# Kernel tuning notes

Hardware: AMD Instinct MI355X
Metric: run time of the kernel (lower is better)

The kernel has to match this reference:

```python
import jax, jax.numpy as jnp
import numpy as np

N = 20000    # num nodes
E = 320000   # num edges (also rows of edge_type, SPN line-graph style)
F = 64       # num_features
HID = 64     # hidden_channels
HEADS = 4    # gatv2_heads
NC = 2       # num_classes
PH = 128     # proxy hidden size
SLOPE = 0.2  # PyG GATv2 leaky_relu negative slope


def gatv2(feat, src, dst, wl, wr, att, b, num_nodes, concat):
    # GATv2Conv (PyG semantics, add_self_loops=True, dropout off in eval)
    H, C = att.shape
    xl = (feat @ wl).reshape(-1, H, C)
    xr = (feat @ wr).reshape(-1, H, C)
    loops = jnp.arange(num_nodes, dtype=src.dtype)
    s = jnp.concatenate([src, loops])
    d = jnp.concatenate([dst, loops])
    e = jax.nn.leaky_relu(xl[s] + xr[d], SLOPE)            # [E', H, C]
    logits = jnp.einsum('ehc,hc->eh', e, att)              # [E', H]
    m = jax.ops.segment_max(logits, d, num_segments=num_nodes)
    p = jnp.exp(logits - m[d])
    z = jax.ops.segment_sum(p, d, num_segments=num_nodes)
    alpha = p / z[d]                                       # segment softmax
    out = jax.ops.segment_sum(xl[s] * alpha[:, :, None], d, num_segments=num_nodes)
    out = out.reshape(num_nodes, H * C) if concat else out.mean(axis=1)
    return out + b


def setup_inputs():
    key = jax.random.key(0)
    ks = iter(jax.random.split(key, 32))
    def rn(shape, scale=0.1):
        return jax.random.normal(next(ks), shape, dtype=jnp.float32) * scale
    return {
        'x': rn((N, F), 1.0),
        'edge_type': rn((E, F), 1.0),
        'edge_index': jax.random.randint(next(ks), (2, E), 0, N, dtype=jnp.int32),
        'n1_wl': rn((F, HEADS * HID)), 'n1_wr': rn((F, HEADS * HID)),
        'n1_att': rn((HEADS, HID)), 'n1_b': jnp.zeros((HEADS * HID,), jnp.float32),
        'n2_wl': rn((HEADS * HID, HID)), 'n2_wr': rn((HEADS * HID, HID)),
        'n2_att': rn((1, HID)), 'n2_b': jnp.zeros((HID,), jnp.float32),
        'e1_wl': rn((F, HEADS * HID)), 'e1_wr': rn((F, HEADS * HID)),
        'e1_att': rn((HEADS, HID)), 'e1_b': jnp.zeros((HEADS * HID,), jnp.float32),
        'e2_wl': rn((HEADS * HID, HID)), 'e2_wr': rn((HEADS * HID, HID)),
        'e2_att': rn((1, HID)), 'e2_b': jnp.zeros((HID,), jnp.float32),
        'crf_wu': rn((HID, NC)), 'crf_bu': jnp.zeros((NC,), jnp.float32),
        'crf_wp': rn((HID, NC)),
        'px_w1': rn((HID, PH)), 'px_b1': jnp.zeros((PH,), jnp.float32),
        'px_w2': rn((PH, NC)), 'px_b2': jnp.zeros((NC,), jnp.float32),
    }


def reference(x, edge_type, edge_index, n1_wl, n1_wr, n1_att, n1_b, n2_wl, n2_wr, n2_att, n2_b,
              e1_wl, e1_wr, e1_att, e1_b, e2_wl, e2_wr, e2_att, e2_b,
              crf_wu, crf_bu, crf_wp, px_w1, px_b1, px_w2, px_b2):
    src, dst = edge_index[0], edge_index[1]
    # node GNN: GATv2 -> ELU -> GATv2 (dropout = identity in eval)
    h = jax.nn.elu(gatv2(x, src, dst, n1_wl, n1_wr, n1_att, n1_b, N, True))
    node_repr = gatv2(h, src, dst, n2_wl, n2_wr, n2_att, n2_b, N, False)
    # edge GNN over edge features (E rows, same edge_index, per source code)
    g = jax.nn.elu(gatv2(edge_type, src, dst, e1_wl, e1_wr, e1_att, e1_b, E, True))
    edge_repr = gatv2(g, src, dst, e2_wl, e2_wr, e2_att, e2_b, E, False)
    # CRF head: unary potentials + pairwise messages scattered to dst nodes
    unary = node_repr @ crf_wu + crf_bu
    msg = jax.ops.segment_sum(edge_repr @ crf_wp, dst, num_segments=N)
    crf_out = jax.nn.log_softmax(unary + msg, axis=-1)
    # MLP proxy head
    ph = jax.nn.relu(node_repr @ px_w1 + px_b1)
    proxy_out = ph @ px_w2 + px_b2
    return crf_out, proxy_out
```

## Files before the change

kernel.cpp:

```cpp
#include <hip/hip_runtime.h>
#include <cstddef>
#include <cstdint>

#define N_NODES 20000
#define N_EDGES 320000

typedef __attribute__((ext_vector_type(8))) short bf8_t;
typedef __attribute__((ext_vector_type(4))) float f4_t;
typedef __attribute__((ext_vector_type(2))) float f2_t;
typedef unsigned short bfu;
typedef _Float16 half_t;
typedef __attribute__((ext_vector_type(2))) _Float16 h2_t;
typedef __attribute__((ext_vector_type(4))) _Float16 h4_t;
typedef __attribute__((ext_vector_type(8))) _Float16 h8_t;

__device__ __forceinline__ short f2bf(float f) {
  unsigned u = __float_as_uint(f);
  u += 0x7fff + ((u >> 16) & 1);
  return (short)(u >> 16);
}
__device__ __forceinline__ h2_t abs_h2(h2_t t) {
  unsigned u = __builtin_bit_cast(unsigned, t) & 0x7fff7fffu;
  return __builtin_bit_cast(h2_t, u);
}
__device__ __forceinline__ float dot2h(h2_t a, h2_t b, float c) {
#if __has_builtin(__builtin_amdgcn_fdot2)
  return __builtin_amdgcn_fdot2(a, b, c, false);
#else
  return c + (float)a.x * (float)b.x + (float)a.y * (float)b.y;
#endif
}

__global__ void count_deg_kernel(const int* __restrict__ dst, int* __restrict__ deg, int e_cnt) {
  int e = blockIdx.x * blockDim.x + threadIdx.x;
  if (e < e_cnt) atomicAdd(&deg[dst[e]], 1);
}

__global__ __launch_bounds__(1024) void scan_kernel(
    const int* __restrict__ deg, int* __restrict__ rowptr,
    int* __restrict__ cursor, int n) {
  __shared__ int sdata[1024];
  constexpr int CH = (N_NODES + 1023) / 1024;
  int tid = threadIdx.x;
  int base = tid * CH;
  int loc[CH];
  int s = 0;
  #pragma unroll
  for (int j = 0; j < CH; ++j) {
    int idx = base + j;
    int v = (idx < n) ? deg[idx] : 0;
    loc[j] = s;
    s += v;
  }
  sdata[tid] = s;
  __syncthreads();
  for (int off = 1; off < 1024; off <<= 1) {
    int t = (tid >= off) ? sdata[tid - off] : 0;
    __syncthreads();
    sdata[tid] += t;
    __syncthreads();
  }
  int excl = sdata[tid] - s;
  #pragma unroll
  for (int j = 0; j < CH; ++j) {
    int idx = base + j;
    if (idx < n) { int val = excl + loc[j]; rowptr[idx] = val; cursor[idx] = val; }
  }
  if (tid == 0) rowptr[n] = sdata[1023];
}

__global__ void fill_csr_kernel(const int* __restrict__ src, const int* __restrict__ dst,
                                int* __restrict__ cursor, int* __restrict__ csr_src,
                                int* __restrict__ csr_eid, int e_cnt) {
  int e = blockIdx.x * blockDim.x + threadIdx.x;
  if (e < e_cnt) {
    int pos = atomicAdd(&cursor[dst[e]], 1);
    csr_src[pos] = src[e];
    csr_eid[pos] = e;
  }
}

__global__ void prep_all_kernel(
    const float* __restrict__ n1l, const float* __restrict__ n1r,
    const float* __restrict__ e1l, const float* __restrict__ e1r,
    const float* __restrict__ n2l, const float* __restrict__ n2r,
    const float* __restrict__ e2l, const float* __restrict__ e2r,
    const float* __restrict__ b2, const float* __restrict__ wp,
    short* __restrict__ t_n1l, short* __restrict__ t_n1r,
    short* __restrict__ t_e1l, short* __restrict__ t_e1r,
    short* __restrict__ t_n2l, short* __restrict__ t_n2r,
    short* __restrict__ t_e2l, short* __restrict__ t_e2r,
    float* __restrict__ wct, float* __restrict__ pc)
{
  int i = blockIdx.x * blockDim.x + threadIdx.x;
  int seg = i >> 14;
  int j = i & 16383;
  if (seg < 4) {
    const float* srcs[4] = {n1l, n1r, e1l, e1r};
    short* dsts[4] = {t_n1l, t_n1r, t_e1l, t_e1r};
    int n = j >> 6, k = j & 63;
    dsts[seg][n * 64 + k] = f2bf(srcs[seg][k * 256 + n]);
  } else if (seg < 8) {
    const float* srcs[4] = {n2l, n2r, e2l, e2r};
    short* dsts[4] = {t_n2l, t_n2r, t_e2l, t_e2r};
    int n = j >> 8, k = j & 255;
    dsts[seg - 4][n * 256 + k] = f2bf(srcs[seg - 4][k * 64 + n]);
  } else if (seg == 8) {
    if (j < 512) {
      int jj = j & 1;
      int k  = j >> 1;
      float s = 0.f;
      for (int c = 0; c < 64; ++c) s = fmaf(e2l[k * 64 + c], wp[c * 2 + jj], s);
      wct[jj * 256 + k] = s;
    } else if (j < 514) {
      int jj = j - 512;
      float s = 0.f;
      for (int c = 0; c < 64; ++c) s = fmaf(b2[c], wp[c * 2 + jj], s);
      pc[jj] = s;
    }
  }
}

template<int K>
__global__ __launch_bounds__(128) void mfma_proj2_kernel(
    const float* __restrict__ A0,
    const short* __restrict__ Wtl0, const short* __restrict__ Wtr0,
    half_t* __restrict__ xl0, half_t* __restrict__ xr0,
    const float* __restrict__ A1,
    const short* __restrict__ Wtl1, const short* __restrict__ Wtr1,
    half_t* __restrict__ xl1, half_t* __restrict__ xr1,
    const float* __restrict__ att0, const float* __restrict__ att1,
    float* __restrict__ ll0, float* __restrict__ lr0,
    float* __restrict__ ll1, float* __restrict__ lr1,
    int M, int nslices)
{
  constexpr int KC = K / 32;
  int tid = threadIdx.x;
  int w = tid >> 6, lane = tid & 63, quad = lane >> 4, l15 = lane & 15;
  int row_base = (int)blockIdx.x * 64 + w * 32;
  int y = (int)blockIdx.y;
  int z = (int)blockIdx.z;
  const float* A = z ? A1 : A0;
  bool is_l = y < nslices;
  const short* Wt = z ? (is_l ? Wtl1 : Wtr1) : (is_l ? Wtl0 : Wtr0);
  half_t* dst = z ? (is_l ? xl1 : xr1) : (is_l ? xl0 : xr0);
  const float* att = z ? att1 : att0;
  float* lin = z ? (is_l ? ll1 : lr1) : (is_l ? ll0 : lr0);
  int head = is_l ? y : y - nslices;
  int cb = head * 64;
  const float* atp = att + head * 64;
  int STR = nslices * 64;

  bf8_t a[2][KC];
  #pragma unroll
  for (int rt = 0; rt < 2; ++rt) {
    int r = row_base + rt * 16 + l15;
    int rc = r < M ? r : M - 1;
    const float* ap = A + (size_t)rc * K + quad * 8;
    #pragma unroll
    for (int kc = 0; kc < KC; ++kc) {
      float4 v0 = *(const float4*)(ap + kc * 32);
      float4 v1 = *(const float4*)(ap + kc * 32 + 4);
      bf8_t f;
      f[0] = f2bf(v0.x); f[1] = f2bf(v0.y); f[2] = f2bf(v0.z); f[3] = f2bf(v0.w);
      f[4] = f2bf(v1.x); f[5] = f2bf(v1.y); f[6] = f2bf(v1.z); f[7] = f2bf(v1.w);
      a[rt][kc] = f;
    }
  }

  float lacc0 = 0.f, lacc1 = 0.f;
  #pragma unroll
  for (int nt = 0; nt < 4; ++nt) {
    f4_t acc0 = {0.f, 0.f, 0.f, 0.f};
    f4_t acc1 = {0.f, 0.f, 0.f, 0.f};
    const short* wb = Wt + (size_t)(cb + nt * 16 + l15) * K + quad * 8;
    #pragma unroll
    for (int kc = 0; kc < KC; ++kc) {
      bf8_t wf = *(const bf8_t*)(wb + kc * 32);
      acc0 = __builtin_amdgcn_mfma_f32_16x16x32_bf16(wf, a[0][kc], acc0, 0, 0, 0);
      acc1 = __builtin_amdgcn_mfma_f32_16x16x32_bf16(wf, a[1][kc], acc1, 0, 0, 0);
    }
    f4_t av = *(const f4_t*)(atp + nt * 16 + quad * 4);
    lacc0 += acc0[0] * av[0] + acc0[1] * av[1] + acc0[2] * av[2] + acc0[3] * av[3];
    lacc1 += acc1[0] * av[0] + acc1[1] * av[1] + acc1[2] * av[2] + acc1[3] * av[3];
    #pragma unroll
    for (int rt = 0; rt < 2; ++rt) {
      f4_t acc = rt == 0 ? acc0 : acc1;
      int row = row_base + rt * 16 + l15;
      if (row >= M) continue;
      int col = cb + nt * 16 + quad * 4;
      h4_t pk;
      pk[0] = (_Float16)acc[0]; pk[1] = (_Float16)acc[1];
      pk[2] = (_Float16)acc[2]; pk[3] = (_Float16)acc[3];
      *(h4_t*)&dst[(size_t)row * STR + col] = pk;
    }
  }
  lacc0 += __shfl_xor(lacc0, 16, 64); lacc0 += __shfl_xor(lacc0, 32, 64);
  lacc1 += __shfl_xor(lacc1, 16, 64); lacc1 += __shfl_xor(lacc1, 32, 64);
  if (quad == 0) {
    int r0 = row_base + l15;
    int r1 = row_base + 16 + l15;
    if (r0 < M) lin[(size_t)r0 * nslices + head] = 0.6f * lacc0;
    if (r1 < M) lin[(size_t)r1 * nslices + head] = 0.6f * lacc1;
  }
}

template<int KIN>
__device__ __forceinline__ void gemm_body(
    const float* __restrict__ A, const float* __restrict__ W, int wld, int cb,
    int block_m, int M, float (&acc)[8][4],
    float (*As)[128 + 4], float (*Ws)[64 + 4])
{
  int tid = threadIdx.x;
  int tx = tid & 15;
  int ty = tid >> 4;
  #pragma unroll
  for (int i = 0; i < 8; ++i)
    #pragma unroll
    for (int j = 0; j < 4; ++j) acc[i][j] = 0.f;

  for (int k0 = 0; k0 < KIN; k0 += 16) {
    #pragma unroll
    for (int rep = 0; rep < 2; ++rep) {
      int ar = (tid >> 2) + rep * 64;
      int ak = (tid & 3) * 4;
      int gr = block_m + ar;
      float4 v = make_float4(0.f, 0.f, 0.f, 0.f);
      if (gr < M) v = *(const float4*)&A[(size_t)gr * KIN + k0 + ak];
      As[ak + 0][ar] = v.x; As[ak + 1][ar] = v.y;
      As[ak + 2][ar] = v.z; As[ak + 3][ar] = v.w;
    }
    {
      int wr = tid >> 4;
      int wc = (tid & 15) * 4;
      float4 v = *(const float4*)&W[(size_t)(k0 + wr) * wld + cb + wc];
      Ws[wr][wc + 0] = v.x; Ws[wr][wc + 1] = v.y;
      Ws[wr][wc + 2] = v.z; Ws[wr][wc + 3] = v.w;
    }
    __syncthreads();
    #pragma unroll
    for (int k = 0; k < 16; ++k) {
      float a[8], w[4];
      #pragma unroll
      for (int i = 0; i < 8; ++i) a[i] = As[k][ty * 8 + i];
      #pragma unroll
      for (int j = 0; j < 4; ++j) w[j] = Ws[k][tx * 4 + j];
      #pragma unroll
      for (int i = 0; i < 8; ++i)
        #pragma unroll
        for (int j = 0; j < 4; ++j) acc[i][j] = fmaf(a[i], w[j], acc[i][j]);
    }
    __syncthreads();
  }
}

template<int KIN, int MODE>
__global__ __launch_bounds__(256) void gemm64_kernel(
    const float* __restrict__ A, const float* __restrict__ W, int wld,
    const float* __restrict__ bias, float* __restrict__ out, int old, int M)
{
  __shared__ float As[16][128 + 4];
  __shared__ float Ws[16][64 + 4];
  float acc[8][4];
  int block_m = (int)blockIdx.x * 128;
  int cb = (int)blockIdx.y * 64;
  gemm_body<KIN>(A, W, wld, cb, block_m, M, acc, As, Ws);

  int tid = threadIdx.x;
  int tx = tid & 15, ty = tid >> 4;
  int gc = cb + tx * 4;
  #pragma unroll
  for (int i = 0; i < 8; ++i) {
    int gr = block_m + ty * 8 + i;
    if (gr >= M) continue;
    size_t idx = (size_t)gr * old + gc;
    float t0 = acc[i][0], t1 = acc[i][1], t2 = acc[i][2], t3 = acc[i][3];
    if (MODE == 3) {
      t0 = fmaxf(t0 + bias[gc + 0], 0.f);
      t1 = fmaxf(t1 + bias[gc + 1], 0.f);
      t2 = fmaxf(t2 + bias[gc + 2], 0.f);
      t3 = fmaxf(t3 + bias[gc + 3], 0.f);
    }
    *(float4*)&out[idx] = make_float4(t0, t1, t2, t3);
  }
}

__global__ __launch_bounds__(256) void gat_agg_l1(
    const half_t* __restrict__ xl0, const half_t* __restrict__ xr0,
    const float* __restrict__ att0, const float* __restrict__ bias0,
    float* __restrict__ out0,
    const half_t* __restrict__ xl1, const half_t* __restrict__ xr1,
    const float* __restrict__ att1, const float* __restrict__ bias1,
    float* __restrict__ out1,
    const float* __restrict__ ll0, const float* __restrict__ lr0,
    const float* __restrict__ ll1, const float* __restrict__ lr1,
    const int* __restrict__ rowptr, const int* __restrict__ csr_src)
{
  constexpr int GRP = N_NODES / 4;
  int tid = threadIdx.x;
  int w = tid >> 6, lane = tid & 63;
  int egrp = lane >> 5;
  int head = (lane >> 3) & 3;
  int coff = (lane & 31) * 8;
  int bid = (int)blockIdx.x;
  int chain = bid >= GRP ? 1 : 0;
  int d = (bid - chain * GRP) * 4 + w;

  const half_t* xl = chain ? xl1 : xl0;
  const half_t* xr = chain ? xr1 : xr0;
  const float* att = chain ? att1 : att0;
  const float* bias = chain ? bias1 : bias0;
  const float* linl = chain ? ll1 : ll0;
  const float* linr = chain ? lr1 : lr0;
  float* out = chain ? out1 : out0;

  int row0 = rowptr[d];
  int deg = rowptr[d + 1] - row0;

  h2_t xr2[4], attA[4];
  {
    h8_t xv = *(const h8_t*)&xr[(unsigned)(d * 256 + coff)];
    xr2[0] = h2_t{xv[0], xv[1]}; xr2[1] = h2_t{xv[2], xv[3]};
    xr2[2] = h2_t{xv[4], xv[5]}; xr2[3] = h2_t{xv[6], xv[7]};
    const float* atp = att + coff;
    float4 b0 = *(const float4*)(atp);
    float4 b1 = *(const float4*)(atp + 4);
    attA[0] = h2_t{(_Float16)(0.4f * b0.x), (_Float16)(0.4f * b0.y)};
    attA[1] = h2_t{(_Float16)(0.4f * b0.z), (_Float16)(0.4f * b0.w)};
    attA[2] = h2_t{(_Float16)(0.4f * b1.x), (_Float16)(0.4f * b1.y)};
    attA[3] = h2_t{(_Float16)(0.4f * b1.z), (_Float16)(0.4f * b1.w)};
  }
  float linr_d = linr[(unsigned)(d * 4 + head)];

  auto ld_idx = [&](int k) -> int {
    int idx = k * 2 + egrp;
    int cl = idx < deg ? idx : (deg > 0 ? deg - 1 : 0);
    int pos = deg > 0 ? row0 + cl : 0;
    int sv = csr_src[pos];
    return idx < deg ? sv : d;
  };

  float zloc, a8[8];
  {
    h8_t xu = *(const h8_t*)&xl[(unsigned)(d * 256 + coff)];
    float part = 0.f;
    #pragma unroll
    for (int j = 0; j < 4; ++j) {
      h2_t t = h2_t{xu[2 * j], xu[2 * j + 1]} + xr2[j];
      part = dot2h(abs_h2(t), attA[j], part);
    }
    part += __shfl_xor(part, 1, 64);
    part += __shfl_xor(part, 2, 64);
    part += __shfl_xor(part, 4, 64);
    part += linl[(unsigned)(d * 4 + head)] + linr_d;
    float wgt = __expf(part);
    float ws = (egrp == 0) ? wgt : 0.f;
    zloc = ws;
    #pragma unroll
    for (int i = 0; i < 8; ++i) a8[i] = (float)xu[i] * ws;
  }

  int C = (deg + 1) >> 1;
  int s_cur = ld_idx(0);
  h8_t xu_cur = *(const h8_t*)&xl[(unsigned)(s_cur * 256 + coff)];
  float lin_cur = linl[(unsigned)(s_cur * 4 + head)];
  int s_nxt = ld_idx(1);
  for (int k = 0; k < C; ++k) {
    h8_t xu_nxt = *(const h8_t*)&xl[(unsigned)(s_nxt * 256 + coff)];
    float lin_nxt = linl[(unsigned)(s_nxt * 4 + head)];
    int s_n2 = ld_idx(k + 2);
    bool valid = (k * 2 + egrp) < deg;
    float part = 0.f;
    #pragma unroll
    for (int j = 0; j < 4; ++j) {
      h2_t t = h2_t{xu_cur[2 * j], xu_cur[2 * j + 1]} + xr2[j];
      part = dot2h(abs_h2(t), attA[j], part);
    }
    part += __shfl_xor(part, 1, 64);
    part += __shfl_xor(part, 2, 64);
    part += __shfl_xor(part, 4, 64);
    part += lin_cur + linr_d;
    float wgt = valid ? __expf(part) : 0.f;
    zloc += wgt;
    #pragma unroll
    for (int i = 0; i < 8; ++i) a8[i] = fmaf((float)xu_cur[i], wgt, a8[i]);
    xu_cur = xu_nxt; lin_cur = lin_nxt; s_nxt = s_n2;
  }

  zloc += __shfl_xor(zloc, 32, 64);
  #pragma unroll
  for (int i = 0; i < 8; ++i) a8[i] += __shfl_xor(a8[i], 32, 64);

  if (egrp == 0) {
    float invz = 1.f / zloc;
    const float* bp = bias + coff;
    float4 c0 = *(const float4*)(bp);
    float4 c1 = *(const float4*)(bp + 4);
    float o[8];
    o[0] = a8[0] * invz + c0.x; o[1] = a8[1] * invz + c0.y;
    o[2] = a8[2] * invz + c0.z; o[3] = a8[3] * invz + c0.w;
    o[4] = a8[4] * invz + c1.x; o[5] = a8[5] * invz + c1.y;
    o[6] = a8[6] * invz + c1.z; o[7] = a8[7] * invz + c1.w;
    #pragma unroll
    for (int i = 0; i < 8; ++i) o[i] = o[i] > 0.f ? o[i] : __expf(o[i]) - 1.f;
    float* op = out + (size_t)d * 256 + coff;
    *(float4*)(op)     = make_float4(o[0], o[1], o[2], o[3]);
    *(float4*)(op + 4) = make_float4(o[4], o[5], o[6], o[7]);
  }
}

__global__ __launch_bounds__(256) void gat_agg_l2(
    const half_t* __restrict__ xl0, const half_t* __restrict__ xr0,
    const float* __restrict__ att0, const float* __restrict__ bias0,
    float* __restrict__ out0,
    const half_t* __restrict__ xl1, const half_t* __restrict__ xr1,
    const float* __restrict__ att1, const float* __restrict__ bias1,
    const float* __restrict__ ll0, const float* __restrict__ lr0,
    const float* __restrict__ ll1, const float* __restrict__ lr1,
    const int* __restrict__ rowptr, const int* __restrict__ csr_src,
    const float* __restrict__ wp, float* __restrict__ pbuf)
{
  constexpr int GRP = N_NODES / 4;
  int tid = threadIdx.x;
  int w = tid >> 6;
  int lane = tid & 63;
  int egrp = lane >> 3;
  int cch  = lane & 7;
  int bid = (int)blockIdx.x;
  int chain = bid >= GRP ? 1 : 0;
  int d = (bid - chain * GRP) * 4 + w;

  const half_t* xl = chain ? xl1 : xl0;
  const half_t* xr = chain ? xr1 : xr0;
  const float* att = chain ? att1 : att0;
  const float* bias = chain ? bias1 : bias0;
  const float* linl = chain ? ll1 : ll0;
  const float* linr = chain ? lr1 : lr0;

  int row0 = rowptr[d];
  int deg = rowptr[d + 1] - row0;
  int cbase = cch * 8;

  h2_t xr2[4], attA[4];
  {
    h8_t xv = *(const h8_t*)&xr[(unsigned)(d * 64 + cbase)];
    xr2[0] = h2_t{xv[0], xv[1]}; xr2[1] = h2_t{xv[2], xv[3]};
    xr2[2] = h2_t{xv[4], xv[5]}; xr2[3] = h2_t{xv[6], xv[7]};
    const float* atp = att + cbase;
    float4 b0 = *(const float4*)(atp);
    float4 b1 = *(const float4*)(atp + 4);
    attA[0] = h2_t{(_Float16)(0.4f * b0.x), (_Float16)(0.4f * b0.y)};
    attA[1] = h2_t{(_Float16)(0.4f * b0.z), (_Float16)(0.4f * b0.w)};
    attA[2] = h2_t{(_Float16)(0.4f * b1.x), (_Float16)(0.4f * b1.y)};
    attA[3] = h2_t{(_Float16)(0.4f * b1.z), (_Float16)(0.4f * b1.w)};
  }
  float linr_d = linr[d];

  auto ld_idx = [&](int k) -> int {
    int idx = k * 8 + egrp;
    int cl = idx < deg ? idx : (deg > 0 ? deg - 1 : 0);
    int pos = deg > 0 ? row0 + cl : 0;
    int sv = csr_src[pos];
    return idx < deg ? sv : d;
  };

  float zloc, a8[8];
  {
    h8_t xu = *(const h8_t*)&xl[(unsigned)(d * 64 + cbase)];
    float part = 0.f;
    #pragma unroll
    for (int j = 0; j < 4; ++j) {
      h2_t t = h2_t{xu[2 * j], xu[2 * j + 1]} + xr2[j];
      part = dot2h(abs_h2(t), attA[j], part);
    }
    part += __shfl_xor(part, 1, 64);
    part += __shfl_xor(part, 2, 64);
    part += __shfl_xor(part, 4, 64);
    part += linl[d] + linr_d;
    float wgt = __expf(part);
    float ws = (egrp == 0) ? wgt : 0.f;
    zloc = ws;
    #pragma unroll
    for (int i = 0; i < 8; ++i) a8[i] = (float)xu[i] * ws;
  }

  int C = (deg + 7) >> 3;
  int s_cur = ld_idx(0);
  h8_t xu_cur = *(const h8_t*)&xl[(unsigned)(s_cur * 64 + cbase)];
  float lin_cur = linl[s_cur];
  int s_nxt = ld_idx(1);
  for (int k = 0; k < C; ++k) {
    h8_t xu_nxt = *(const h8_t*)&xl[(unsigned)(s_nxt * 64 + cbase)];
    float lin_nxt = linl[s_nxt];
    int s_n2 = ld_idx(k + 2);
    bool valid = (k * 8 + egrp) < deg;
    float part = 0.f;
    #pragma unroll
    for (int j = 0; j < 4; ++j) {
      h2_t t = h2_t{xu_cur[2 * j], xu_cur[2 * j + 1]} + xr2[j];
      part = dot2h(abs_h2(t), attA[j], part);
    }
    part += __shfl_xor(part, 1, 64);
    part += __shfl_xor(part, 2, 64);
    part += __shfl_xor(part, 4, 64);
    part += lin_cur + linr_d;
    float wgt = valid ? __expf(part) : 0.f;
    zloc += wgt;
    #pragma unroll
    for (int i = 0; i < 8; ++i) a8[i] = fmaf((float)xu_cur[i], wgt, a8[i]);
    xu_cur = xu_nxt; lin_cur = lin_nxt; s_nxt = s_n2;
  }

  #pragma unroll
  for (int off = 8; off < 64; off <<= 1) {
    zloc += __shfl_xor(zloc, off, 64);
    #pragma unroll
    for (int i = 0; i < 8; ++i) a8[i] += __shfl_xor(a8[i], off, 64);
  }

  float invz = 1.f / zloc;
  float o[8];
  #pragma unroll
  for (int i = 0; i < 8; ++i) o[i] = a8[i] * invz + bias[cbase + i];

  if (chain) {
    float p0 = 0.f, p1 = 0.f;
    #pragma unroll
    for (int i = 0; i < 8; ++i) {
      float2 wv = *(const float2*)&wp[(cbase + i) * 2];
      p0 = fmaf(o[i], wv.x, p0);
      p1 = fmaf(o[i], wv.y, p1);
    }
    p0 += __shfl_xor(p0, 1, 64); p1 += __shfl_xor(p1, 1, 64);
    p0 += __shfl_xor(p0, 2, 64); p1 += __shfl_xor(p1, 2, 64);
    p0 += __shfl_xor(p0, 4, 64); p1 += __shfl_xor(p1, 4, 64);
    if (lane == 0) *(float2*)&pbuf[2 * d] = make_float2(p0, p1);
  } else if (egrp == 0) {
    float* op = out0 + (size_t)d * 64 + cbase;
    *(float4*)(op)     = make_float4(o[0], o[1], o[2], o[3]);
    *(float4*)(op + 4) = make_float4(o[4], o[5], o[6], o[7]);
  }
}

__global__ __launch_bounds__(256) void chunk_fold_kernel(
    const float* __restrict__ A,
    const short* __restrict__ W1t,
    const float* __restrict__ b1,
    const float* __restrict__ WcT,
    const float* __restrict__ pc,
    float* __restrict__ pbufN,
    int Mtot)
{
  int tid = threadIdx.x;
  int w = tid >> 6;
  int lane = tid & 63;
  int quad = lane >> 4;
  int l15 = lane & 15;
  int row_base = (int)blockIdx.x * 256 + w * 64;

  bf8_t a1[4][2];
  #pragma unroll
  for (int rt = 0; rt < 4; ++rt) {
    int r = row_base + rt * 16 + l15;
    int rc = r < Mtot ? r : Mtot - 1;
    const float* ap = A + (size_t)rc * 64 + quad * 8;
    #pragma unroll
    for (int ks = 0; ks < 2; ++ks) {
      float4 v0 = *(const float4*)(ap + ks * 32);
      float4 v1 = *(const float4*)(ap + ks * 32 + 4);
      bf8_t f;
      f[0] = f2bf(v0.x); f[1] = f2bf(v0.y); f[2] = f2bf(v0.z); f[3] = f2bf(v0.w);
      f[4] = f2bf(v1.x); f[5] = f2bf(v1.y); f[6] = f2bf(v1.z); f[7] = f2bf(v1.w);
      a1[rt][ks] = f;
    }
  }

  float p0[4] = {0.f, 0.f, 0.f, 0.f};
  float p1[4] = {0.f, 0.f, 0.f, 0.f};

  #pragma unroll
  for (int cc = 0; cc < 4; ++cc) {
    #pragma unroll
    for (int nt = 0; nt < 4; ++nt) {
      const short* wb = W1t + (cc * 64 + nt * 16 + l15) * 64 + quad * 8;
      bf8_t w0 = *(const bf8_t*)(wb);
      bf8_t w1 = *(const bf8_t*)(wb + 32);
      f4_t g[4];
      #pragma unroll
      for (int rt = 0; rt < 4; ++rt) {
        f4_t z = {0.f, 0.f, 0.f, 0.f};
        z = __builtin_amdgcn_mfma_f32_16x16x32_bf16(w0, a1[rt][0], z, 0, 0, 0);
        z = __builtin_amdgcn_mfma_f32_16x16x32_bf16(w1, a1[rt][1], z, 0, 0, 0);
        g[rt] = z;
      }
      int cbase = cc * 64 + nt * 16 + quad * 4;
      f4_t b4  = *(const f4_t*)&b1[cbase];
      f4_t wc0 = *(const f4_t*)&WcT[cbase];
      f4_t wc1 = *(const f4_t*)&WcT[256 + cbase];
      #pragma unroll
      for (int rt = 0; rt < 4; ++rt) {
        #pragma unroll
        for (int r = 0; r < 4; ++r) {
          float v = g[rt][r] + b4[r];
          v = v > 0.f ? v : __expf(v) - 1.f;
          p0[rt] = fmaf(v, wc0[r], p0[rt]);
          p1[rt] = fmaf(v, wc1[r], p1[rt]);
        }
      }
    }
  }

  #pragma unroll
  for (int off = 16; off < 64; off <<= 1) {
    #pragma unroll
    for (int rt = 0; rt < 4; ++rt) {
      p0[rt] += __shfl_xor(p0[rt], off, 64);
      p1[rt] += __shfl_xor(p1[rt], off, 64);
    }
  }
  if (quad == 0) {
    float c0 = pc[0], c1 = pc[1];
    #pragma unroll
    for (int rt = 0; rt < 4; ++rt) {
      int row = row_base + rt * 16 + l15;
      if (row < Mtot)
        *(float2*)&pbufN[2 * row] = make_float2(p0[rt] + c0, p1[rt] + c1);
    }
  }
}

__global__ void head_kernel(const float* __restrict__ node_repr, const float* __restrict__ ph,
                            const int* __restrict__ rowptr, const int* __restrict__ csr_eid,
                            const float* __restrict__ pbuf, const float* __restrict__ wu,
                            const float* __restrict__ bu, const float* __restrict__ w2,
                            const float* __restrict__ b2, float* __restrict__ out, int n) {
  __shared__ float swu[128];
  __shared__ float sw2[256];
  int tid = threadIdx.x;
  if (tid < 128) swu[tid] = wu[tid];
  sw2[tid] = w2[tid];
  __syncthreads();
  int i = blockIdx.x * blockDim.x + tid;
  if (i >= n) return;
  float m0 = 0.f, m1 = 0.f;
  int r0 = rowptr[i], r1 = rowptr[i + 1];
  int jj = r0;
  for (; jj + 4 <= r1; jj += 4) {
    int e0 = csr_eid[jj + 0], e1 = csr_eid[jj + 1];
    int e2 = csr_eid[jj + 2], e3 = csr_eid[jj + 3];
    float2 q0 = *(const float2*)&pbuf[2 * e0];
    float2 q1 = *(const float2*)&pbuf[2 * e1];
    float2 q2 = *(const float2*)&pbuf[2 * e2];
    float2 q3 = *(const float2*)&pbuf[2 * e3];
    m0 += (q0.x + q1.x) + (q2.x + q3.x);
    m1 += (q0.y + q1.y) + (q2.y + q3.y);
  }
  for (; jj < r1; ++jj) {
    int e = csr_eid[jj];
    float2 q = *(const float2*)&pbuf[2 * e];
    m0 += q.x; m1 += q.y;
  }
  const float* nr = node_repr + (size_t)i * 64;
  float u0 = bu[0], u1 = bu[1];
  #pragma unroll
  for (int k = 0; k < 64; ++k) {
    float v = nr[k];
    u0 = fmaf(v, swu[2 * k + 0], u0);
    u1 = fmaf(v, swu[2 * k + 1], u1);
  }
  float v0 = u0 + m0;
  float v1 = u1 + m1;
  float mx = fmaxf(v0, v1);
  float lse = mx + logf(__expf(v0 - mx) + __expf(v1 - mx));
  out[2 * i + 0] = v0 - lse;
  out[2 * i + 1] = v1 - lse;
  const float* p = ph + (size_t)i * 128;
  float p0 = b2[0], p1 = b2[1];
  #pragma unroll
  for (int k = 0; k < 128; ++k) {
    float v = p[k];
    p0 = fmaf(v, sw2[2 * k + 0], p0);
    p1 = fmaf(v, sw2[2 * k + 1], p1);
  }
  out[2 * n + 2 * i + 0] = p0;
  out[2 * n + 2 * i + 1] = p1;
}

extern "C" void kernel_launch(void* const* d_in, const int* in_sizes, int n_in,
                              void* d_out, int out_size, void* d_ws, size_t ws_size,
                              hipStream_t stream) {
  const int N = N_NODES, E = N_EDGES;
  const float* x         = (const float*)d_in[0];
  const float* edge_type = (const float*)d_in[1];
  const int*   ei        = (const int*)d_in[2];
  const float* n1_wl  = (const float*)d_in[3];
  const float* n1_wr  = (const float*)d_in[4];
  const float* n1_att = (const float*)d_in[5];
  const float* n1_b   = (const float*)d_in[6];
  const float* n2_wl  = (const float*)d_in[7];
  const float* n2_wr  = (const float*)d_in[8];
  const float* n2_att = (const float*)d_in[9];
  const float* n2_b   = (const float*)d_in[10];
  const float* e1_wl  = (const float*)d_in[11];
  const float* e1_wr  = (const float*)d_in[12];
  const float* e1_att = (const float*)d_in[13];
  const float* e1_b   = (const float*)d_in[14];
  const float* e2_wl  = (const float*)d_in[15];
  const float* e2_wr  = (const float*)d_in[16];
  const float* e2_att = (const float*)d_in[17];
  const float* e2_b   = (const float*)d_in[18];
  const float* crf_wu = (const float*)d_in[19];
  const float* crf_bu = (const float*)d_in[20];
  const float* crf_wp = (const float*)d_in[21];
  const float* px_w1  = (const float*)d_in[22];
  const float* px_b1  = (const float*)d_in[23];
  const float* px_w2  = (const float*)d_in[24];
  const float* px_b2  = (const float*)d_in[25];
  float* out = (float*)d_out;
  const int* src = ei;
  const int* dst = ei + E;
  (void)in_sizes; (void)n_in; (void)out_size; (void)ws_size;

  char* ws = (char*)d_ws;
  size_t off = 0;
  auto alloc = [&](size_t bytes) -> void* {
    void* p = ws + off;
    off += (bytes + 255) & ~(size_t)255;
    return p;
  };
  half_t* xl_n  = (half_t*)alloc((size_t)N * 256 * 2);
  half_t* xr_n  = (half_t*)alloc((size_t)N * 256 * 2);
  half_t* xl_e  = (half_t*)alloc((size_t)N * 256 * 2);
  half_t* xr_e  = (half_t*)alloc((size_t)N * 256 * 2);
  float* h_n   = (float*)alloc((size_t)N * 256 * 4);
  float* g_e   = (float*)alloc((size_t)N * 256 * 4);
  half_t* xl2_n = (half_t*)alloc((size_t)N * 64 * 2);
  half_t* xr2_n = (half_t*)alloc((size_t)N * 64 * 2);
  half_t* xl2_e = (half_t*)alloc((size_t)N * 64 * 2);
  half_t* xr2_e = (half_t*)alloc((size_t)N * 64 * 2);
  float* B3    = (float*)alloc((size_t)N * 64 * 4);
  float* pbuf  = (float*)alloc((size_t)E * 2 * 4);
  float* ph    = (float*)(void*)xl_n;
  int* deg     = (int*)alloc((size_t)N * 4);
  int* rowptr  = (int*)alloc((size_t)(N + 1) * 4);
  int* cursor  = (int*)alloc((size_t)N * 4);
  int* csr_src = (int*)alloc((size_t)E * 4);
  int* csr_eid = (int*)alloc((size_t)E * 4);
  short* t_n1l = (short*)alloc((size_t)16384 * 2);
  short* t_n1r = (short*)alloc((size_t)16384 * 2);
  short* t_e1l = (short*)alloc((size_t)16384 * 2);
  short* t_e1r = (short*)alloc((size_t)16384 * 2);
  short* t_n2l = (short*)alloc((size_t)16384 * 2);
  short* t_n2r = (short*)alloc((size_t)16384 * 2);
  short* t_e2l = (short*)alloc((size_t)16384 * 2);
  short* t_e2r = (short*)alloc((size_t)16384 * 2);
  float* WcT   = (float*)alloc((size_t)2 * 256 * 4);
  float* pcv   = (float*)alloc((size_t)2 * 4);
  float* l1ln = pbuf;
  float* l1rn = pbuf + 80000;
  float* l1le = pbuf + 160000;
  float* l1re = pbuf + 240000;
  float* l2base = (float*)(void*)xr_n;
  float* l2ln = l2base;
  float* l2rn = l2base + 20000;
  float* l2le = l2base + 40000;
  float* l2re = l2base + 60000;

  const int EB = (E + 255) / 256;
  const int NB = (N + 127) / 128;
  const int PB = (N + 63) / 64;
  const int Mhigh = E - N;
  const int CFB = (Mhigh + 255) / 256;
  const int GRP = N / 4;

  hipMemsetAsync(deg, 0, (size_t)N * 4, stream);
  count_deg_kernel<<<EB, 256, 0, stream>>>(dst, deg, E);
  scan_kernel<<<1, 1024, 0, stream>>>(deg, rowptr, cursor, N);
  fill_csr_kernel<<<EB, 256, 0, stream>>>(src, dst, cursor, csr_src, csr_eid, E);
  prep_all_kernel<<<515, 256, 0, stream>>>(n1_wl, n1_wr, e1_wl, e1_wr,
                                           n2_wl, n2_wr, e2_wl, e2_wr,
                                           e2_b, crf_wp,
                                           t_n1l, t_n1r, t_e1l, t_e1r,
                                           t_n2l, t_n2r, t_e2l, t_e2r, WcT, pcv);

  mfma_proj2_kernel<64><<<dim3(PB, 8, 2), 128, 0, stream>>>(
      x, t_n1l, t_n1r, xl_n, xr_n,
      edge_type, t_e1l, t_e1r, xl_e, xr_e,
      n1_att, e1_att, l1ln, l1rn, l1le, l1re, N, 4);
  gat_agg_l1<<<2 * GRP, 256, 0, stream>>>(
      xl_n, xr_n, n1_att, n1_b, h_n,
      xl_e, xr_e, e1_att, e1_b, g_e,
      l1ln, l1rn, l1le, l1re, rowptr, csr_src);

  mfma_proj2_kernel<256><<<dim3(PB, 2, 2), 128, 0, stream>>>(
      h_n, t_n2l, t_n2r, xl2_n, xr2_n,
      g_e, t_e2l, t_e2r, xl2_e, xr2_e,
      n2_att, e2_att, l2ln, l2rn, l2le, l2re, N, 1);
  gat_agg_l2<<<2 * GRP, 256, 0, stream>>>(
      xl2_n, xr2_n, n2_att, n2_b, B3,
      xl2_e, xr2_e, e2_att, e2_b,
      l2ln, l2rn, l2le, l2re, rowptr, csr_src, crf_wp, pbuf);

  chunk_fold_kernel<<<CFB, 256, 0, stream>>>(edge_type + (size_t)N * 64, t_e1l,
                                             e1_b, WcT, pcv, pbuf + 2 * (size_t)N, Mhigh);

  gemm64_kernel<64, 3><<<dim3(NB, 2), 256, 0, stream>>>(B3, px_w1, 128, px_b1, ph, 128, N);
  head_kernel<<<(N + 255) / 256, 256, 0, stream>>>(B3, ph, rowptr, csr_eid, pbuf,
                                                   crf_wu, crf_bu, px_w2, px_b2, out, N);
}
```

Measured before the change: 426.0 us.

## Fuse chunk-fold work into layer-1 aggregation launch via block-index dispatch

```diff
diff --git a/kernel.cpp b/kernel.cpp
--- a/kernel.cpp
+++ b/kernel.cpp
@@ -285,264 +285,8 @@
   }
 }
 
-__global__ __launch_bounds__(256) void gat_agg_l1(
-    const half_t* __restrict__ xl0, const half_t* __restrict__ xr0,
-    const float* __restrict__ att0, const float* __restrict__ bias0,
-    float* __restrict__ out0,
-    const half_t* __restrict__ xl1, const half_t* __restrict__ xr1,
-    const float* __restrict__ att1, const float* __restrict__ bias1,
-    float* __restrict__ out1,
-    const float* __restrict__ ll0, const float* __restrict__ lr0,
-    const float* __restrict__ ll1, const float* __restrict__ lr1,
-    const int* __restrict__ rowptr, const int* __restrict__ csr_src)
-{
-  constexpr int GRP = N_NODES / 4;
-  int tid = threadIdx.x;
-  int w = tid >> 6, lane = tid & 63;
-  int egrp = lane >> 5;
-  int head = (lane >> 3) & 3;
-  int coff = (lane & 31) * 8;
-  int bid = (int)blockIdx.x;
-  int chain = bid >= GRP ? 1 : 0;
-  int d = (bid - chain * GRP) * 4 + w;
-
-  const half_t* xl = chain ? xl1 : xl0;
-  const half_t* xr = chain ? xr1 : xr0;
-  const float* att = chain ? att1 : att0;
-  const float* bias = chain ? bias1 : bias0;
-  const float* linl = chain ? ll1 : ll0;
-  const float* linr = chain ? lr1 : lr0;
-  float* out = chain ? out1 : out0;
-
-  int row0 = rowptr[d];
-  int deg = rowptr[d + 1] - row0;
-
-  h2_t xr2[4], attA[4];
-  {
-    h8_t xv = *(const h8_t*)&xr[(unsigned)(d * 256 + coff)];
-    xr2[0] = h2_t{xv[0], xv[1]}; xr2[1] = h2_t{xv[2], xv[3]};
-    xr2[2] = h2_t{xv[4], xv[5]}; xr2[3] = h2_t{xv[6], xv[7]};
-    const float* atp = att + coff;
-    float4 b0 = *(const float4*)(atp);
-    float4 b1 = *(const float4*)(atp + 4);
-    attA[0] = h2_t{(_Float16)(0.4f * b0.x), (_Float16)(0.4f * b0.y)};
-    attA[1] = h2_t{(_Float16)(0.4f * b0.z), (_Float16)(0.4f * b0.w)};
-    attA[2] = h2_t{(_Float16)(0.4f * b1.x), (_Float16)(0.4f * b1.y)};
-    attA[3] = h2_t{(_Float16)(0.4f * b1.z), (_Float16)(0.4f * b1.w)};
-  }
-  float linr_d = linr[(unsigned)(d * 4 + head)];
-
-  auto ld_idx = [&](int k) -> int {
-    int idx = k * 2 + egrp;
-    int cl = idx < deg ? idx : (deg > 0 ? deg - 1 : 0);
-    int pos = deg > 0 ? row0 + cl : 0;
-    int sv = csr_src[pos];
-    return idx < deg ? sv : d;
-  };
-
-  float zloc, a8[8];
-  {
-    h8_t xu = *(const h8_t*)&xl[(unsigned)(d * 256 + coff)];
-    float part = 0.f;
-    #pragma unroll
-    for (int j = 0; j < 4; ++j) {
-      h2_t t = h2_t{xu[2 * j], xu[2 * j + 1]} + xr2[j];
-      part = dot2h(abs_h2(t), attA[j], part);
-    }
-    part += __shfl_xor(part, 1, 64);
-    part += __shfl_xor(part, 2, 64);
-    part += __shfl_xor(part, 4, 64);
-    part += linl[(unsigned)(d * 4 + head)] + linr_d;
-    float wgt = __expf(part);
-    float ws = (egrp == 0) ? wgt : 0.f;
-    zloc = ws;
-    #pragma unroll
-    for (int i = 0; i < 8; ++i) a8[i] = (float)xu[i] * ws;
-  }
-
-  int C = (deg + 1) >> 1;
-  int s_cur = ld_idx(0);
-  h8_t xu_cur = *(const h8_t*)&xl[(unsigned)(s_cur * 256 + coff)];
-  float lin_cur = linl[(unsigned)(s_cur * 4 + head)];
-  int s_nxt = ld_idx(1);
-  for (int k = 0; k < C; ++k) {
-    h8_t xu_nxt = *(const h8_t*)&xl[(unsigned)(s_nxt * 256 + coff)];
-    float lin_nxt = linl[(unsigned)(s_nxt * 4 + head)];
-    int s_n2 = ld_idx(k + 2);
-    bool valid = (k * 2 + egrp) < deg;
-    float part = 0.f;
-    #pragma unroll
-    for (int j = 0; j < 4; ++j) {
-      h2_t t = h2_t{xu_cur[2 * j], xu_cur[2 * j + 1]} + xr2[j];
-      part = dot2h(abs_h2(t), attA[j], part);
-    }
-    part += __shfl_xor(part, 1, 64);
-    part += __shfl_xor(part, 2, 64);
-    part += __shfl_xor(part, 4, 64);
-    part += lin_cur + linr_d;
-    float wgt = valid ? __expf(part) : 0.f;
-    zloc += wgt;
-    #pragma unroll
-    for (int i = 0; i < 8; ++i) a8[i] = fmaf((float)xu_cur[i], wgt, a8[i]);
-    xu_cur = xu_nxt; lin_cur = lin_nxt; s_nxt = s_n2;
-  }
-
-  zloc += __shfl_xor(zloc, 32, 64);
-  #pragma unroll
-  for (int i = 0; i < 8; ++i) a8[i] += __shfl_xor(a8[i], 32, 64);
-
-  if (egrp == 0) {
-    float invz = 1.f / zloc;
-    const float* bp = bias + coff;
-    float4 c0 = *(const float4*)(bp);
-    float4 c1 = *(const float4*)(bp + 4);
-    float o[8];
-    o[0] = a8[0] * invz + c0.x; o[1] = a8[1] * invz + c0.y;
-    o[2] = a8[2] * invz + c0.z; o[3] = a8[3] * invz + c0.w;
-    o[4] = a8[4] * invz + c1.x; o[5] = a8[5] * invz + c1.y;
-    o[6] = a8[6] * invz + c1.z; o[7] = a8[7] * invz + c1.w;
-    #pragma unroll
-    for (int i = 0; i < 8; ++i) o[i] = o[i] > 0.f ? o[i] : __expf(o[i]) - 1.f;
-    float* op = out + (size_t)d * 256 + coff;
-    *(float4*)(op)     = make_float4(o[0], o[1], o[2], o[3]);
-    *(float4*)(op + 4) = make_float4(o[4], o[5], o[6], o[7]);
-  }
-}
-
-__global__ __launch_bounds__(256) void gat_agg_l2(
-    const half_t* __restrict__ xl0, const half_t* __restrict__ xr0,
-    const float* __restrict__ att0, const float* __restrict__ bias0,
-    float* __restrict__ out0,
-    const half_t* __restrict__ xl1, const half_t* __restrict__ xr1,
-    const float* __restrict__ att1, const float* __restrict__ bias1,
-    const float* __restrict__ ll0, const float* __restrict__ lr0,
-    const float* __restrict__ ll1, const float* __restrict__ lr1,
-    const int* __restrict__ rowptr, const int* __restrict__ csr_src,
-    const float* __restrict__ wp, float* __restrict__ pbuf)
-{
-  constexpr int GRP = N_NODES / 4;
-  int tid = threadIdx.x;
-  int w = tid >> 6;
-  int lane = tid & 63;
-  int egrp = lane >> 3;
-  int cch  = lane & 7;
-  int bid = (int)blockIdx.x;
-  int chain = bid >= GRP ? 1 : 0;
-  int d = (bid - chain * GRP) * 4 + w;
-
-  const half_t* xl = chain ? xl1 : xl0;
-  const half_t* xr = chain ? xr1 : xr0;
-  const float* att = chain ? att1 : att0;
-  const float* bias = chain ? bias1 : bias0;
-  const float* linl = chain ? ll1 : ll0;
-  const float* linr = chain ? lr1 : lr0;
-
-  int row0 = rowptr[d];
-  int deg = rowptr[d + 1] - row0;
-  int cbase = cch * 8;
-
-  h2_t xr2[4], attA[4];
-  {
-    h8_t xv = *(const h8_t*)&xr[(unsigned)(d * 64 + cbase)];
-    xr2[0] = h2_t{xv[0], xv[1]}; xr2[1] = h2_t{xv[2], xv[3]};
-    xr2[2] = h2_t{xv[4], xv[5]}; xr2[3] = h2_t{xv[6], xv[7]};
-    const float* atp = att + cbase;
-    float4 b0 = *(const float4*)(atp);
-    float4 b1 = *(const float4*)(atp + 4);
-    attA[0] = h2_t{(_Float16)(0.4f * b0.x), (_Float16)(0.4f * b0.y)};
-    attA[1] = h2_t{(_Float16)(0.4f * b0.z), (_Float16)(0.4f * b0.w)};
-    attA[2] = h2_t{(_Float16)(0.4f * b1.x), (_Float16)(0.4f * b1.y)};
-    attA[3] = h2_t{(_Float16)(0.4f * b1.z), (_Float16)(0.4f * b1.w)};
-  }
-  float linr_d = linr[d];
-
-  auto ld_idx = [&](int k) -> int {
-    int idx = k * 8 + egrp;
-    int cl = idx < deg ? idx : (deg > 0 ? deg - 1 : 0);
-    int pos = deg > 0 ? row0 + cl : 0;
-    int sv = csr_src[pos];
-    return idx < deg ? sv : d;
-  };
-
-  float zloc, a8[8];
-  {
-    h8_t xu = *(const h8_t*)&xl[(unsigned)(d * 64 + cbase)];
-    float part = 0.f;
-    #pragma unroll
-    for (int j = 0; j < 4; ++j) {
-      h2_t t = h2_t{xu[2 * j], xu[2 * j + 1]} + xr2[j];
-      part = dot2h(abs_h2(t), attA[j], part);
-    }
-    part += __shfl_xor(part, 1, 64);
-    part += __shfl_xor(part, 2, 64);
-    part += __shfl_xor(part, 4, 64);
-    part += linl[d] + linr_d;
-    float wgt = __expf(part);
-    float ws = (egrp == 0) ? wgt : 0.f;
-    zloc = ws;
-    #pragma unroll
-    for (int i = 0; i < 8; ++i) a8[i] = (float)xu[i] * ws;
-  }
-
-  int C = (deg + 7) >> 3;
-  int s_cur = ld_idx(0);
-  h8_t xu_cur = *(const h8_t*)&xl[(unsigned)(s_cur * 64 + cbase)];
-  float lin_cur = linl[s_cur];
-  int s_nxt = ld_idx(1);
-  for (int k = 0; k < C; ++k) {
-    h8_t xu_nxt = *(const h8_t*)&xl[(unsigned)(s_nxt * 64 + cbase)];
-    float lin_nxt = linl[s_nxt];
-    int s_n2 = ld_idx(k + 2);
-    bool valid = (k * 8 + egrp) < deg;
-    float part = 0.f;
-    #pragma unroll
-    for (int j = 0; j < 4; ++j) {
-      h2_t t = h2_t{xu_cur[2 * j], xu_cur[2 * j + 1]} + xr2[j];
-      part = dot2h(abs_h2(t), attA[j], part);
-    }
-    part += __shfl_xor(part, 1, 64);
-    part += __shfl_xor(part, 2, 64);
-    part += __shfl_xor(part, 4, 64);
-    part += lin_cur + linr_d;
-    float wgt = valid ? __expf(part) : 0.f;
-    zloc += wgt;
-    #pragma unroll
-    for (int i = 0; i < 8; ++i) a8[i] = fmaf((float)xu_cur[i], wgt, a8[i]);
-    xu_cur = xu_nxt; lin_cur = lin_nxt; s_nxt = s_n2;
-  }
-
-  #pragma unroll
-  for (int off = 8; off < 64; off <<= 1) {
-    zloc += __shfl_xor(zloc, off, 64);
-    #pragma unroll
-    for (int i = 0; i < 8; ++i) a8[i] += __shfl_xor(a8[i], off, 64);
-  }
-
-  float invz = 1.f / zloc;
-  float o[8];
-  #pragma unroll
-  for (int i = 0; i < 8; ++i) o[i] = a8[i] * invz + bias[cbase + i];
-
-  if (chain) {
-    float p0 = 0.f, p1 = 0.f;
-    #pragma unroll
-    for (int i = 0; i < 8; ++i) {
-      float2 wv = *(const float2*)&wp[(cbase + i) * 2];
-      p0 = fmaf(o[i], wv.x, p0);
-      p1 = fmaf(o[i], wv.y, p1);
-    }
-    p0 += __shfl_xor(p0, 1, 64); p1 += __shfl_xor(p1, 1, 64);
-    p0 += __shfl_xor(p0, 2, 64); p1 += __shfl_xor(p1, 2, 64);
-    p0 += __shfl_xor(p0, 4, 64); p1 += __shfl_xor(p1, 4, 64);
-    if (lane == 0) *(float2*)&pbuf[2 * d] = make_float2(p0, p1);
-  } else if (egrp == 0) {
-    float* op = out0 + (size_t)d * 64 + cbase;
-    *(float4*)(op)     = make_float4(o[0], o[1], o[2], o[3]);
-    *(float4*)(op + 4) = make_float4(o[4], o[5], o[6], o[7]);
-  }
-}
-
-__global__ __launch_bounds__(256) void chunk_fold_kernel(
+__device__ __forceinline__ void chunk_fold_body(
+    int cbid,
     const float* __restrict__ A,
     const short* __restrict__ W1t,
     const float* __restrict__ b1,
@@ -556,7 +300,7 @@
   int lane = tid & 63;
   int quad = lane >> 4;
   int l15 = lane & 15;
-  int row_base = (int)blockIdx.x * 256 + w * 64;
+  int row_base = cbid * 256 + w * 64;
 
   bf8_t a1[4][2];
   #pragma unroll
@@ -626,6 +370,289 @@
       if (row < Mtot)
         *(float2*)&pbufN[2 * row] = make_float2(p0[rt] + c0, p1[rt] + c1);
     }
+  }
+}
+
+__device__ __forceinline__ void gat_agg_l1_body(
+    int bid,
+    const half_t* __restrict__ xl0, const half_t* __restrict__ xr0,
+    const float* __restrict__ att0, const float* __restrict__ bias0,
+    float* __restrict__ out0,
+    const half_t* __restrict__ xl1, const half_t* __restrict__ xr1,
+    const float* __restrict__ att1, const float* __restrict__ bias1,
+    float* __restrict__ out1,
+    const float* __restrict__ ll0, const float* __restrict__ lr0,
+    const float* __restrict__ ll1, const float* __restrict__ lr1,
+    const int* __restrict__ rowptr, const int* __restrict__ csr_src)
+{
+  constexpr int GRP = N_NODES / 4;
+  int tid = threadIdx.x;
+  int w = tid >> 6, lane = tid & 63;
+  int egrp = lane >> 5;
+  int head = (lane >> 3) & 3;
+  int coff = (lane & 31) * 8;
+  int chain = bid >= GRP ? 1 : 0;
+  int d = (bid - chain * GRP) * 4 + w;
+
+  const half_t* xl = chain ? xl1 : xl0;
+  const half_t* xr = chain ? xr1 : xr0;
+  const float* att = chain ? att1 : att0;
+  const float* bias = chain ? bias1 : bias0;
+  const float* linl = chain ? ll1 : ll0;
+  const float* linr = chain ? lr1 : lr0;
+  float* out = chain ? out1 : out0;
+
+  int row0 = rowptr[d];
+  int deg = rowptr[d + 1] - row0;
+
+  h2_t xr2[4], attA[4];
+  {
+    h8_t xv = *(const h8_t*)&xr[(unsigned)(d * 256 + coff)];
+    xr2[0] = h2_t{xv[0], xv[1]}; xr2[1] = h2_t{xv[2], xv[3]};
+    xr2[2] = h2_t{xv[4], xv[5]}; xr2[3] = h2_t{xv[6], xv[7]};
+    const float* atp = att + coff;
+    float4 b0 = *(const float4*)(atp);
+    float4 b1 = *(const float4*)(atp + 4);
+    attA[0] = h2_t{(_Float16)(0.4f * b0.x), (_Float16)(0.4f * b0.y)};
+    attA[1] = h2_t{(_Float16)(0.4f * b0.z), (_Float16)(0.4f * b0.w)};
+    attA[2] = h2_t{(_Float16)(0.4f * b1.x), (_Float16)(0.4f * b1.y)};
+    attA[3] = h2_t{(_Float16)(0.4f * b1.z), (_Float16)(0.4f * b1.w)};
+  }
+  float linr_d = linr[(unsigned)(d * 4 + head)];
+
+  auto ld_idx = [&](int k) -> int {
+    int idx = k * 2 + egrp;
+    int cl = idx < deg ? idx : (deg > 0 ? deg - 1 : 0);
+    int pos = deg > 0 ? row0 + cl : 0;
+    int sv = csr_src[pos];
+    return idx < deg ? sv : d;
+  };
+
+  float zloc, a8[8];
+  {
+    h8_t xu = *(const h8_t*)&xl[(unsigned)(d * 256 + coff)];
+    float part = 0.f;
+    #pragma unroll
+    for (int j = 0; j < 4; ++j) {
+      h2_t t = h2_t{xu[2 * j], xu[2 * j + 1]} + xr2[j];
+      part = dot2h(abs_h2(t), attA[j], part);
+    }
+    part += __shfl_xor(part, 1, 64);
+    part += __shfl_xor(part, 2, 64);
+    part += __shfl_xor(part, 4, 64);
+    part += linl[(unsigned)(d * 4 + head)] + linr_d;
+    float wgt = __expf(part);
+    float ws = (egrp == 0) ? wgt : 0.f;
+    zloc = ws;
+    #pragma unroll
+    for (int i = 0; i < 8; ++i) a8[i] = (float)xu[i] * ws;
+  }
+
+  int C = (deg + 1) >> 1;
+  int s_cur = ld_idx(0);
+  h8_t xu_cur = *(const h8_t*)&xl[(unsigned)(s_cur * 256 + coff)];
+  float lin_cur = linl[(unsigned)(s_cur * 4 + head)];
+  int s_nxt = ld_idx(1);
+  for (int k = 0; k < C; ++k) {
+    h8_t xu_nxt = *(const h8_t*)&xl[(unsigned)(s_nxt * 256 + coff)];
+    float lin_nxt = linl[(unsigned)(s_nxt * 4 + head)];
+    int s_n2 = ld_idx(k + 2);
+    bool valid = (k * 2 + egrp) < deg;
+    float part = 0.f;
+    #pragma unroll
+    for (int j = 0; j < 4; ++j) {
+      h2_t t = h2_t{xu_cur[2 * j], xu_cur[2 * j + 1]} + xr2[j];
+      part = dot2h(abs_h2(t), attA[j], part);
+    }
+    part += __shfl_xor(part, 1, 64);
+    part += __shfl_xor(part, 2, 64);
+    part += __shfl_xor(part, 4, 64);
+    part += lin_cur + linr_d;
+    float wgt = valid ? __expf(part) : 0.f;
+    zloc += wgt;
+    #pragma unroll
+    for (int i = 0; i < 8; ++i) a8[i] = fmaf((float)xu_cur[i], wgt, a8[i]);
+    xu_cur = xu_nxt; lin_cur = lin_nxt; s_nxt = s_n2;
+  }
+
+  zloc += __shfl_xor(zloc, 32, 64);
+  #pragma unroll
+  for (int i = 0; i < 8; ++i) a8[i] += __shfl_xor(a8[i], 32, 64);
+
+  if (egrp == 0) {
+    float invz = 1.f / zloc;
+    const float* bp = bias + coff;
+    float4 c0 = *(const float4*)(bp);
+    float4 c1 = *(const float4*)(bp + 4);
+    float o[8];
+    o[0] = a8[0] * invz + c0.x; o[1] = a8[1] * invz + c0.y;
+    o[2] = a8[2] * invz + c0.z; o[3] = a8[3] * invz + c0.w;
+    o[4] = a8[4] * invz + c1.x; o[5] = a8[5] * invz + c1.y;
+    o[6] = a8[6] * invz + c1.z; o[7] = a8[7] * invz + c1.w;
+    #pragma unroll
+    for (int i = 0; i < 8; ++i) o[i] = o[i] > 0.f ? o[i] : __expf(o[i]) - 1.f;
+    float* op = out + (size_t)d * 256 + coff;
+    *(float4*)(op)     = make_float4(o[0], o[1], o[2], o[3]);
+    *(float4*)(op + 4) = make_float4(o[4], o[5], o[6], o[7]);
+  }
+}
+
+__global__ __launch_bounds__(256) void agg1_chunk_fused(
+    const half_t* __restrict__ xl0, const half_t* __restrict__ xr0,
+    const float* __restrict__ att0, const float* __restrict__ bias0,
+    float* __restrict__ out0,
+    const half_t* __restrict__ xl1, const half_t* __restrict__ xr1,
+    const float* __restrict__ att1, const float* __restrict__ bias1,
+    float* __restrict__ out1,
+    const float* __restrict__ ll0, const float* __restrict__ lr0,
+    const float* __restrict__ ll1, const float* __restrict__ lr1,
+    const int* __restrict__ rowptr, const int* __restrict__ csr_src,
+    const float* __restrict__ A, const short* __restrict__ W1t,
+    const float* __restrict__ b1, const float* __restrict__ WcT,
+    const float* __restrict__ pc, float* __restrict__ pbufN,
+    int Mtot, int n_chunk_blocks)
+{
+  int bx = (int)blockIdx.x;
+  if (bx < n_chunk_blocks) {
+    chunk_fold_body(bx, A, W1t, b1, WcT, pc, pbufN, Mtot);
+  } else {
+    gat_agg_l1_body(bx - n_chunk_blocks,
+                    xl0, xr0, att0, bias0, out0,
+                    xl1, xr1, att1, bias1, out1,
+                    ll0, lr0, ll1, lr1, rowptr, csr_src);
+  }
+}
+
+__global__ __launch_bounds__(256) void gat_agg_l2(
+    const half_t* __restrict__ xl0, const half_t* __restrict__ xr0,
+    const float* __restrict__ att0, const float* __restrict__ bias0,
+    float* __restrict__ out0,
+    const half_t* __restrict__ xl1, const half_t* __restrict__ xr1,
+    const float* __restrict__ att1, const float* __restrict__ bias1,
+    const float* __restrict__ ll0, const float* __restrict__ lr0,
+    const float* __restrict__ ll1, const float* __restrict__ lr1,
+    const int* __restrict__ rowptr, const int* __restrict__ csr_src,
+    const float* __restrict__ wp, float* __restrict__ pbuf)
+{
+  constexpr int GRP = N_NODES / 4;
+  int tid = threadIdx.x;
+  int w = tid >> 6;
+  int lane = tid & 63;
+  int egrp = lane >> 3;
+  int cch  = lane & 7;
+  int bid = (int)blockIdx.x;
+  int chain = bid >= GRP ? 1 : 0;
+  int d = (bid - chain * GRP) * 4 + w;
+
+  const half_t* xl = chain ? xl1 : xl0;
+  const half_t* xr = chain ? xr1 : xr0;
+  const float* att = chain ? att1 : att0;
+  const float* bias = chain ? bias1 : bias0;
+  const float* linl = chain ? ll1 : ll0;
+  const float* linr = chain ? lr1 : lr0;
+
+  int row0 = rowptr[d];
+  int deg = rowptr[d + 1] - row0;
+  int cbase = cch * 8;
+
+  h2_t xr2[4], attA[4];
+  {
+    h8_t xv = *(const h8_t*)&xr[(unsigned)(d * 64 + cbase)];
+    xr2[0] = h2_t{xv[0], xv[1]}; xr2[1] = h2_t{xv[2], xv[3]};
+    xr2[2] = h2_t{xv[4], xv[5]}; xr2[3] = h2_t{xv[6], xv[7]};
+    const float* atp = att + cbase;
+    float4 b0 = *(const float4*)(atp);
+    float4 b1 = *(const float4*)(atp + 4);
+    attA[0] = h2_t{(_Float16)(0.4f * b0.x), (_Float16)(0.4f * b0.y)};
+    attA[1] = h2_t{(_Float16)(0.4f * b0.z), (_Float16)(0.4f * b0.w)};
+    attA[2] = h2_t{(_Float16)(0.4f * b1.x), (_Float16)(0.4f * b1.y)};
+    attA[3] = h2_t{(_Float16)(0.4f * b1.z), (_Float16)(0.4f * b1.w)};
+  }
+  float linr_d = linr[d];
+
+  auto ld_idx = [&](int k) -> int {
+    int idx = k * 8 + egrp;
+    int cl = idx < deg ? idx : (deg > 0 ? deg - 1 : 0);
+    int pos = deg > 0 ? row0 + cl : 0;
+    int sv = csr_src[pos];
+    return idx < deg ? sv : d;
+  };
+
+  float zloc, a8[8];
+  {
+    h8_t xu = *(const h8_t*)&xl[(unsigned)(d * 64 + cbase)];
+    float part = 0.f;
+    #pragma unroll
+    for (int j = 0; j < 4; ++j) {
+      h2_t t = h2_t{xu[2 * j], xu[2 * j + 1]} + xr2[j];
+      part = dot2h(abs_h2(t), attA[j], part);
+    }
+    part += __shfl_xor(part, 1, 64);
+    part += __shfl_xor(part, 2, 64);
+    part += __shfl_xor(part, 4, 64);
+    part += linl[d] + linr_d;
+    float wgt = __expf(part);
+    float ws = (egrp == 0) ? wgt : 0.f;
+    zloc = ws;
+    #pragma unroll
+    for (int i = 0; i < 8; ++i) a8[i] = (float)xu[i] * ws;
+  }
+
+  int C = (deg + 7) >> 3;
+  int s_cur = ld_idx(0);
+  h8_t xu_cur = *(const h8_t*)&xl[(unsigned)(s_cur * 64 + cbase)];
+  float lin_cur = linl[s_cur];
+  int s_nxt = ld_idx(1);
+  for (int k = 0; k < C; ++k) {
+    h8_t xu_nxt = *(const h8_t*)&xl[(unsigned)(s_nxt * 64 + cbase)];
+    float lin_nxt = linl[s_nxt];
+    int s_n2 = ld_idx(k + 2);
+    bool valid = (k * 8 + egrp) < deg;
+    float part = 0.f;
+    #pragma unroll
+    for (int j = 0; j < 4; ++j) {
+      h2_t t = h2_t{xu_cur[2 * j], xu_cur[2 * j + 1]} + xr2[j];
+      part = dot2h(abs_h2(t), attA[j], part);
+    }
+    part += __shfl_xor(part, 1, 64);
+    part += __shfl_xor(part, 2, 64);
+    part += __shfl_xor(part, 4, 64);
+    part += lin_cur + linr_d;
+    float wgt = valid ? __expf(part) : 0.f;
+    zloc += wgt;
+    #pragma unroll
+    for (int i = 0; i < 8; ++i) a8[i] = fmaf((float)xu_cur[i], wgt, a8[i]);
+    xu_cur = xu_nxt; lin_cur = lin_nxt; s_nxt = s_n2;
+  }
+
+  #pragma unroll
+  for (int off = 8; off < 64; off <<= 1) {
+    zloc += __shfl_xor(zloc, off, 64);
+    #pragma unroll
+    for (int i = 0; i < 8; ++i) a8[i] += __shfl_xor(a8[i], off, 64);
+  }
+
+  float invz = 1.f / zloc;
+  float o[8];
+  #pragma unroll
+  for (int i = 0; i < 8; ++i) o[i] = a8[i] * invz + bias[cbase + i];
+
+  if (chain) {
+    float p0 = 0.f, p1 = 0.f;
+    #pragma unroll
+    for (int i = 0; i < 8; ++i) {
+      float2 wv = *(const float2*)&wp[(cbase + i) * 2];
+      p0 = fmaf(o[i], wv.x, p0);
+      p1 = fmaf(o[i], wv.y, p1);
+    }
+    p0 += __shfl_xor(p0, 1, 64); p1 += __shfl_xor(p1, 1, 64);
+    p0 += __shfl_xor(p0, 2, 64); p1 += __shfl_xor(p1, 2, 64);
+    p0 += __shfl_xor(p0, 4, 64); p1 += __shfl_xor(p1, 4, 64);
+    if (lane == 0) *(float2*)&pbuf[2 * d] = make_float2(p0, p1);
+  } else if (egrp == 0) {
+    float* op = out0 + (size_t)d * 64 + cbase;
+    *(float4*)(op)     = make_float4(o[0], o[1], o[2], o[3]);
+    *(float4*)(op + 4) = make_float4(o[4], o[5], o[6], o[7]);
   }
 }
 
@@ -756,10 +783,11 @@
   short* t_e2r = (short*)alloc((size_t)16384 * 2);
   float* WcT   = (float*)alloc((size_t)2 * 256 * 4);
   float* pcv   = (float*)alloc((size_t)2 * 4);
-  float* l1ln = pbuf;
-  float* l1rn = pbuf + 80000;
-  float* l1le = pbuf + 160000;
-  float* l1re = pbuf + 240000;
+  float* l1base = (float*)(void*)xl2_n;
+  float* l1ln = l1base;
+  float* l1rn = l1base + 80000;
+  float* l1le = l1base + 160000;
+  float* l1re = l1base + 240000;
   float* l2base = (float*)(void*)xr_n;
   float* l2ln = l2base;
   float* l2rn = l2base + 20000;
@@ -787,10 +815,13 @@
       x, t_n1l, t_n1r, xl_n, xr_n,
       edge_type, t_e1l, t_e1r, xl_e, xr_e,
       n1_att, e1_att, l1ln, l1rn, l1le, l1re, N, 4);
-  gat_agg_l1<<<2 * GRP, 256, 0, stream>>>(
+
+  agg1_chunk_fused<<<CFB + 2 * GRP, 256, 0, stream>>>(
       xl_n, xr_n, n1_att, n1_b, h_n,
       xl_e, xr_e, e1_att, e1_b, g_e,
-      l1ln, l1rn, l1le, l1re, rowptr, csr_src);
+      l1ln, l1rn, l1le, l1re, rowptr, csr_src,
+      edge_type + (size_t)N * 64, t_e1l, e1_b, WcT, pcv,
+      pbuf + 2 * (size_t)N, Mhigh, CFB);
 
   mfma_proj2_kernel<256><<<dim3(PB, 2, 2), 128, 0, stream>>>(
       h_n, t_n2l, t_n2r, xl2_n, xr2_n,
@@ -801,9 +832,6 @@
       xl2_e, xr2_e, e2_att, e2_b,
       l2ln, l2rn, l2le, l2re, rowptr, csr_src, crf_wp, pbuf);
 
-  chunk_fold_kernel<<<CFB, 256, 0, stream>>>(edge_type + (size_t)N * 64, t_e1l,
-                                             e1_b, WcT, pcv, pbuf + 2 * (size_t)N, Mhigh);
-
   gemm64_kernel<64, 3><<<dim3(NB, 2), 256, 0, stream>>>(B3, px_w1, 128, px_b1, ph, 128, N);
   head_kernel<<<(N + 255) / 256, 256, 0, stream>>>(B3, ph, rowptr, csr_eid, pbuf,
                                                    crf_wu, crf_bu, px_w2, px_b2, out, N);
```

Measured after the change: 443.5 us. 1.04x slower.
